# Optimization experiments

Hardware: AMD Instinct MI355X
Metric: run time of the kernel (lower is better)

Reference implementation:

```python
import jax, jax.numpy as jnp
import numpy as np

GRID_SIZE = 20
GRID_MIN, GRID_MAX = -2.0, 2.0
SIGMA = (GRID_MAX - GRID_MIN) / (GRID_SIZE - 1)  # RBF width = grid spacing


def setup_inputs() -> dict:
    key = jax.random.key(0)
    k1, k2, k3 = jax.random.split(key, 3)
    batch, in_features, out_features = 4096, 1024, 1024
    x = jax.random.normal(k1, (batch, in_features), dtype=jnp.float32)
    # glorot-scale initializations for faithfulness to keras glorot_uniform magnitude
    lim_b = np.sqrt(6.0 / (in_features + out_features))
    base_weight = jax.random.uniform(k2, (in_features, out_features), jnp.float32, -lim_b, lim_b)
    lim_s = np.sqrt(6.0 / (in_features * GRID_SIZE + out_features))
    spline_weight = jax.random.uniform(k3, (in_features, GRID_SIZE, out_features), jnp.float32, -lim_s, lim_s)
    mu = jnp.linspace(GRID_MIN, GRID_MAX, GRID_SIZE, dtype=jnp.float32)
    return {"x": x, "base_weight": base_weight, "spline_weight": spline_weight, "mu": mu}


def reference(x, base_weight, spline_weight, mu):
    # base path: SiLU(x) @ W_base
    base_out = jnp.einsum('bi,io->bo', jax.nn.silu(x), base_weight)
    # RBF basis expansion: [b, i, g]
    diff = (x[..., None] - mu) / SIGMA
    basis = jnp.exp(-(diff * diff))
    spline_out = jnp.einsum('big,igo->bo', basis, spline_weight)
    return base_out + spline_out
```

## Files before the change

kernel.cpp:

```cpp
#include <hip/hip_runtime.h>
#include <hip/hip_bf16.h>
#include <stdint.h>


typedef short short8 __attribute__((ext_vector_type(8)));
typedef __bf16 bf16x8 __attribute__((ext_vector_type(8)));
typedef float f32x4 __attribute__((ext_vector_type(4)));
typedef unsigned int u32;

__device__ __forceinline__ unsigned short f2bf(float f) {
  __hip_bfloat16 h = __float2bfloat16(f);
  return __builtin_bit_cast(unsigned short, h);
}

__device__ __forceinline__ void gload_lds16(const unsigned short* g, unsigned short* l) {
  __builtin_amdgcn_global_load_lds(
      (const __attribute__((address_space(1))) u32*)(const void*)g,
      (__attribute__((address_space(3))) u32*)(void*)l, 16, 0, 0);
}


__global__ void prep_silu(const float* __restrict__ x, unsigned short* __restrict__ A1) {
  int g = blockIdx.x * 256 + threadIdx.x;
  const float4* x4 = reinterpret_cast<const float4*>(x);
  float4 a = x4[g * 2], b = x4[g * 2 + 1];
  float v[8] = {a.x, a.y, a.z, a.w, b.x, b.y, b.z, b.w};
  union { unsigned short u[8]; short8 v8; } o;
#pragma unroll
  for (int j = 0; j < 8; ++j) {
    float s = v[j] / (1.f + __expf(-v[j]));
    o.u[j] = f2bf(s);
  }
  *reinterpret_cast<short8*>(&A1[(size_t)g * 8]) = o.v8;
}

__global__ void prep_basis(const float* __restrict__ x, unsigned short* __restrict__ A2,
                           int i0, int L) {
  int g = blockIdx.x * 256 + threadIdx.x;
  int e0 = g * 8;
  int b = e0 / L;
  int k0 = e0 - b * L;
  const float* xr = x + (size_t)b * 1024 + i0;
  union { unsigned short u[8]; short8 v8; } o;
#pragma unroll
  for (int j = 0; j < 8; ++j) {
    int k = k0 + j;
    int il = (int)(((unsigned)k * 104858u) >> 21);
    int gg = k - il * 20;
    float xv = xr[il];
    float d = (xv + 2.0f) * 4.75f - (float)gg;
    o.u[j] = f2bf(__expf(-d * d));
  }
  *reinterpret_cast<short8*>(&A2[(size_t)b * L + k0]) = o.v8;
}

__global__ void prep_wt(const float* __restrict__ W, unsigned short* __restrict__ Bt, int Kp) {
  __shared__ unsigned short tile[64][72];
  int tiles_k = Kp >> 6;
  int bk = blockIdx.x % tiles_k, bn = blockIdx.x / tiles_k;
  int t = threadIdx.x;
  int lr = t >> 4;
  int lc = (t & 15) * 4;
#pragma unroll
  for (int r = 0; r < 4; ++r) {
    int row = r * 16 + lr;
    float4 v = *reinterpret_cast<const float4*>(&W[(size_t)(bk * 64 + row) * 1024 + bn * 64 + lc]);
    tile[row][lc + 0] = f2bf(v.x);
    tile[row][lc + 1] = f2bf(v.y);
    tile[row][lc + 2] = f2bf(v.z);
    tile[row][lc + 3] = f2bf(v.w);
  }
  __syncthreads();
  int nr = t >> 3;
  int kc = (t & 7) * 8;
#pragma unroll
  for (int r = 0; r < 2; ++r) {
    int n = r * 32 + nr;
    union { unsigned short u[8]; short8 v8; } o;
#pragma unroll
    for (int j = 0; j < 8; ++j) o.u[j] = tile[kc + j][n];
    *reinterpret_cast<short8*>(&Bt[(size_t)(bn * 64 + n) * Kp + bk * 64 + kc]) = o.v8;
  }
}

__global__ void add_kernel(float* __restrict__ out, const float* __restrict__ part, int n4) {
  int i = blockIdx.x * 256 + threadIdx.x;
  int stride = gridDim.x * 256;
  for (; i < n4; i += stride) {
    float4 a = reinterpret_cast<float4*>(out)[i];
    float4 b = reinterpret_cast<const float4*>(part)[i];
    a.x += b.x; a.y += b.y; a.z += b.z; a.w += b.w;
    reinterpret_cast<float4*>(out)[i] = a;
  }
}

template <bool SPLIT>
__global__ __launch_bounds__(256, 2) void gemm_bf16(
    const unsigned short* __restrict__ A, int lda,
    const unsigned short* __restrict__ Bt, int ldb,
    float* __restrict__ C0, float* __restrict__ C1, int Kz) {
  const int tid = threadIdx.x;
  const int wid = tid >> 6, lane = tid & 63;

  const int cpx = gridDim.x >> 3;
  const int wg = (blockIdx.x & 7) * cpx + (blockIdx.x >> 3);
  const int mtile = wg & 31;
  const int ntile = (wg >> 5) & 7;
  const int z = SPLIT ? (wg >> 8) : 0;
  const int brow = mtile * 128, bcol = ntile * 128;
  const int kbase = z * Kz;

  __shared__ __align__(16) unsigned short As[128 * 64];
  __shared__ __align__(16) unsigned short Bs[128 * 64];

  const int srow = wid * 32 + (lane >> 3);
  const int scol = (lane & 7) * 8;
  const unsigned short* aptr = A + (size_t)(brow + srow) * lda + kbase + scol;
  const unsigned short* bptr = Bt + (size_t)(bcol + srow) * ldb + kbase + scol;
  unsigned short* lA = &As[wid * 2048];
  unsigned short* lB = &Bs[wid * 2048];

  const int wr = wid >> 1, wc = wid & 1;
  const int fr = lane & 15;
  const int fk = (lane >> 4) * 8;

  f32x4 acc[4][4] = {};

  for (int kt = 0; kt < Kz; kt += 64) {
#pragma unroll
    for (int c = 0; c < 4; ++c)
      gload_lds16(aptr + (size_t)(c * 8) * lda, lA + c * 512);
#pragma unroll
    for (int c = 0; c < 4; ++c)
      gload_lds16(bptr + (size_t)(c * 8) * ldb, lB + c * 512);
    aptr += 64;
    bptr += 64;
    __syncthreads();
#pragma unroll
    for (int ks = 0; ks < 2; ++ks) {
      bf16x8 af[4], bfr[4];
#pragma unroll
      for (int m = 0; m < 4; ++m)
        af[m] = __builtin_bit_cast(
            bf16x8, *reinterpret_cast<const short8*>(
                        &As[(wr * 64 + m * 16 + fr) * 64 + ks * 32 + fk]));
#pragma unroll
      for (int n = 0; n < 4; ++n)
        bfr[n] = __builtin_bit_cast(
            bf16x8, *reinterpret_cast<const short8*>(
                        &Bs[(wc * 64 + n * 16 + fr) * 64 + ks * 32 + fk]));
#pragma unroll
      for (int m = 0; m < 4; ++m)
#pragma unroll
        for (int n = 0; n < 4; ++n)
          acc[m][n] = __builtin_amdgcn_mfma_f32_16x16x32_bf16(af[m], bfr[n], acc[m][n], 0, 0, 0);
    }
    __syncthreads();
  }

  float* C = (SPLIT && z) ? C1 : C0;
  const bool accflag = SPLIT && (z == 1);
  const int r0 = brow + wr * 64 + (lane >> 4) * 4;
  const int c0 = bcol + wc * 64 + (lane & 15);
#pragma unroll
  for (int m = 0; m < 4; ++m)
#pragma unroll
    for (int n = 0; n < 4; ++n)
#pragma unroll
      for (int j = 0; j < 4; ++j) {
        size_t idx = (size_t)(r0 + m * 16 + j) * 1024 + (c0 + n * 16);
        float v = acc[m][n][j];
        if (accflag)
          C[idx] += v;
        else
          C[idx] = v;
      }
}


extern "C" void kernel_launch(void* const* d_in, const int* in_sizes, int n_in,
                              void* d_out, int out_size, void* d_ws, size_t ws_size,
                              hipStream_t stream) {
  (void)in_sizes; (void)n_in; (void)out_size;
  const float* x = (const float*)d_in[0];
  const float* Wb = (const float*)d_in[1];
  const float* Ws = (const float*)d_in[2];
  float* out = (float*)d_out;
  char* ws = (char*)d_ws;

  const size_t A1_off = 0;
  const size_t W1t_off = 8388608;
  const size_t Cp_off = W1t_off + 2097152;
  const size_t dyn_off = Cp_off + 16777216;
  unsigned short* A1  = (unsigned short*)(ws + A1_off);
  unsigned short* W1t = (unsigned short*)(ws + W1t_off);
  float*          Cp  = (float*)(ws + Cp_off);

  int npass = 16;
  for (int np = 2; np <= 16; np <<= 1) {
    size_t CI = 1024 / np;
    size_t need = dyn_off + 4096ull * CI * 20 * 2 + CI * 20 * 1024 * 2;
    if (need <= ws_size) { npass = np; break; }
  }
  const int CI = 1024 / npass;
  const int Kp = CI * 20;
  const int Kz = Kp / 2;
  unsigned short* A2  = (unsigned short*)(ws + dyn_off);
  unsigned short* W2t = (unsigned short*)(ws + dyn_off + 4096ull * CI * 20 * 2);

  prep_silu<<<2048, 256, 0, stream>>>(x, A1);
  prep_wt<<<256, 256, 0, stream>>>(Wb, W1t, 1024);
  gemm_bf16<false><<<256, 256, 0, stream>>>(A1, 1024, W1t, 1024, out, nullptr, 1024);

  for (int p = 0; p < npass; ++p) {
    const int nb_basis = 4096 * Kp / 8 / 256;
    prep_basis<<<nb_basis, 256, 0, stream>>>(x, A2, p * CI, Kp);
    prep_wt<<<(Kp / 64) * 16, 256, 0, stream>>>(Ws + (size_t)p * Kp * 1024, W2t, Kp);
    gemm_bf16<true><<<512, 256, 0, stream>>>(A2, Kp, W2t, Kp, Cp, out, Kz);
    add_kernel<<<2048, 256, 0, stream>>>(out, Cp, 1024 * 1024);
  }
}
```

Baseline: 504.6 us.

## Replace split-K partial buffer and add kernel with 4-way atomic accumulation

The spline GEMM now splits K four ways across 1024 workgroups, and each split accumulates straight into the output with float atomicAdd. This removes the partial-sum buffer and the separate add kernel on every pass. Launch bounds rise to 4 waves per SIMD to allow more resident blocks. In exchange there are many more atomic global writes, summation order becomes nondeterministic, and the higher occupancy target may limit registers for the accumulators.

```diff
diff --git a/kernel.cpp b/kernel.cpp
--- a/kernel.cpp
+++ b/kernel.cpp
@@ -83,22 +83,11 @@
   }
 }
 
-__global__ void add_kernel(float* __restrict__ out, const float* __restrict__ part, int n4) {
-  int i = blockIdx.x * 256 + threadIdx.x;
-  int stride = gridDim.x * 256;
-  for (; i < n4; i += stride) {
-    float4 a = reinterpret_cast<float4*>(out)[i];
-    float4 b = reinterpret_cast<const float4*>(part)[i];
-    a.x += b.x; a.y += b.y; a.z += b.z; a.w += b.w;
-    reinterpret_cast<float4*>(out)[i] = a;
-  }
-}
-
-template <bool SPLIT>
-__global__ __launch_bounds__(256, 2) void gemm_bf16(
+template <bool ATOMIC>
+__global__ __launch_bounds__(256, 4) void gemm_bf16(
     const unsigned short* __restrict__ A, int lda,
     const unsigned short* __restrict__ Bt, int ldb,
-    float* __restrict__ C0, float* __restrict__ C1, int Kz) {
+    float* __restrict__ C, int Kz) {
   const int tid = threadIdx.x;
   const int wid = tid >> 6, lane = tid & 63;
 
@@ -106,7 +95,7 @@
   const int wg = (blockIdx.x & 7) * cpx + (blockIdx.x >> 3);
   const int mtile = wg & 31;
   const int ntile = (wg >> 5) & 7;
-  const int z = SPLIT ? (wg >> 8) : 0;
+  const int z = wg >> 8;
   const int brow = mtile * 128, bcol = ntile * 128;
   const int kbase = z * Kz;
 
@@ -158,8 +147,6 @@
     __syncthreads();
   }
 
-  float* C = (SPLIT && z) ? C1 : C0;
-  const bool accflag = SPLIT && (z == 1);
   const int r0 = brow + wr * 64 + (lane >> 4) * 4;
   const int c0 = bcol + wc * 64 + (lane & 15);
 #pragma unroll
@@ -170,8 +157,8 @@
       for (int j = 0; j < 4; ++j) {
         size_t idx = (size_t)(r0 + m * 16 + j) * 1024 + (c0 + n * 16);
         float v = acc[m][n][j];
-        if (accflag)
-          C[idx] += v;
+        if (ATOMIC)
+          atomicAdd(&C[idx], v);
         else
           C[idx] = v;
       }
@@ -190,11 +177,9 @@
 
   const size_t A1_off = 0;
   const size_t W1t_off = 8388608;
-  const size_t Cp_off = W1t_off + 2097152;
-  const size_t dyn_off = Cp_off + 16777216;
+  const size_t dyn_off = W1t_off + 2097152;
   unsigned short* A1  = (unsigned short*)(ws + A1_off);
   unsigned short* W1t = (unsigned short*)(ws + W1t_off);
-  float*          Cp  = (float*)(ws + Cp_off);
 
   int npass = 16;
   for (int np = 2; np <= 16; np <<= 1) {
@@ -204,19 +189,18 @@
   }
   const int CI = 1024 / npass;
   const int Kp = CI * 20;
-  const int Kz = Kp / 2;
+  const int Kz = Kp / 4;
   unsigned short* A2  = (unsigned short*)(ws + dyn_off);
   unsigned short* W2t = (unsigned short*)(ws + dyn_off + 4096ull * CI * 20 * 2);
 
   prep_silu<<<2048, 256, 0, stream>>>(x, A1);
   prep_wt<<<256, 256, 0, stream>>>(Wb, W1t, 1024);
-  gemm_bf16<false><<<256, 256, 0, stream>>>(A1, 1024, W1t, 1024, out, nullptr, 1024);
+  gemm_bf16<false><<<256, 256, 0, stream>>>(A1, 1024, W1t, 1024, out, 1024);
 
   for (int p = 0; p < npass; ++p) {
     const int nb_basis = 4096 * Kp / 8 / 256;
     prep_basis<<<nb_basis, 256, 0, stream>>>(x, A2, p * CI, Kp);
     prep_wt<<<(Kp / 64) * 16, 256, 0, stream>>>(Ws + (size_t)p * Kp * 1024, W2t, Kp);
-    gemm_bf16<true><<<512, 256, 0, stream>>>(A2, Kp, W2t, Kp, Cp, out, Kz);
-    add_kernel<<<2048, 256, 0, stream>>>(out, Cp, 1024 * 1024);
-  }
-}
+    gemm_bf16<true><<<1024, 256, 0, stream>>>(A2, Kp, W2t, Kp, out, Kz);
+  }
+}
```

Measured after the change: 474.9 us. 1.06x faster.
